# Optimization experiments

Measured on AMD Instinct MI355X. Metric: run time of the kernel, lower is better.

The kernel has to match this reference:

```python
import jax, jax.numpy as jnp
import numpy as np

jax.config.update("jax_enable_x64", True)

HLB_LVL_MAX = 20
HLB_LVL = 5
HLB_SHIFT = True
HLB_MAX = 2 ** HLB_LVL_MAX                      # 1048576
HLB_BIAS = (2 ** (HLB_LVL_MAX - HLB_LVL) - 1) if HLB_SHIFT else 0   # 32767
NUM_BITS = HLB_LVL_MAX + (1 if HLB_SHIFT else 0)  # 21 bits per axis, 63 total -> int64


def hilbert_encode3d(grd, num_bits):
    """Skilling's AxesToTranspose + bit interleave: 3D grid coords -> Hilbert order.
    grd: [..., 3] int64, coords < 2**num_bits. Returns int64 [...].
    Fixed-trip-count Python loops over bits (unrolled at trace time, ~21 iters)."""
    nd = 3
    x = [grd[..., i] for i in range(nd)]
    M = 1 << (num_bits - 1)
    # Inverse undo excess work
    Q = M
    while Q > 1:
        P = Q - 1
        for i in range(nd):
            cond = (x[i] & Q) != 0
            t = (x[0] ^ x[i]) & P
            new_x0 = jnp.where(cond, x[0] ^ P, x[0] ^ t)   # invert low bits of x0, or exchange
            new_xi = jnp.where(cond, x[i], x[i] ^ t)
            x[0] = new_x0
            if i != 0:
                x[i] = new_xi
        Q >>= 1
    # Gray encode
    for i in range(1, nd):
        x[i] = x[i] ^ x[i - 1]
    t = jnp.zeros_like(x[0])
    Q = M
    while Q > 1:
        t = jnp.where((x[nd - 1] & Q) != 0, t ^ (Q - 1), t)
        Q >>= 1
    for i in range(nd):
        x[i] = x[i] ^ t
    # Interleave bits of the transposed coords (x[0] most significant at each level)
    h = jnp.zeros_like(x[0])
    for b in range(num_bits):
        for i in range(nd):
            bit = (x[i] >> b) & 1
            h = h | (bit << (b * nd + (nd - 1 - i)))
    return h


def setup_inputs() -> dict:
    key = jax.random.key(0)
    z = jax.random.normal(key, (32, 131072, 3), dtype=jnp.float32)
    return {"z": z}


def reference(z):
    z = z.astype(jnp.float64)
    z_ce = z.mean(axis=1, keepdims=True)                                  # [B,1,3]
    r = jnp.sqrt(jnp.max(jnp.sum((z - z_ce) ** 2, axis=2), axis=1))       # [B]
    z_r = r[:, None, None] + 1e-6                                          # [B,1,1]
    z_nm = (z - z_ce + z_r) / (2.0 * z_r)                                  # normalized to ~[0,1]
    grd_idx = (HLB_MAX * z_nm).astype(jnp.int64) + HLB_BIAS                # quantize (trunc toward 0)
    hlb_ord = hilbert_encode3d(grd_idx, NUM_BITS)                          # [B,N] int64
    idx_pa = jnp.argsort(hlb_ord, axis=1)                                  # permutation along curve
    idx_re = jnp.argsort(idx_pa, axis=1)                                   # inverse permutation
    return idx_pa, idx_re
```

## Files before the change

kernel.cpp:

```cpp
#include <hip/hip_runtime.h>

typedef unsigned int u32;
typedef unsigned long long u64;
typedef unsigned short u16;

#define NB 32
#define NP 131072
#define THREADS 256
#define STHREADS 1024
#define RADIX 256
#define PASSES 6

#define SBPB 16
#define STILE 8192
#define SIPT 8
#define EBPB 64
#define ETILE 2048
#define EIPT 8


__device__ __forceinline__ u64 spread3(u32 v) {
    u64 x = (u64)(v & 0x1FFFFFu);
    x = (x | (x << 32)) & 0x001F00000000FFFFull;
    x = (x | (x << 16)) & 0x001F0000FF0000FFull;
    x = (x | (x << 8))  & 0x100F00F00F00F00Full;
    x = (x | (x << 4))  & 0x10C30C30C30C30C3ull;
    x = (x | (x << 2))  & 0x1249249249249249ull;
    return x;
}

__device__ __forceinline__ u64 hilbert3d(u32 x0, u32 x1, u32 x2) {
    #pragma unroll
    for (int q = 20; q >= 3; --q) {
        u32 Q = 1u << q, P = Q - 1u;
        if (x0 & Q) x0 ^= P;
        u32 t = (x0 ^ x1) & P;
        if (x1 & Q) { x0 ^= P; } else { x0 ^= t; x1 ^= t; }
        t = (x0 ^ x2) & P;
        if (x2 & Q) { x0 ^= P; } else { x0 ^= t; x2 ^= t; }
    }
    x1 ^= x0;
    x2 ^= x1;
    u32 y = x2;
    y ^= y >> 1; y ^= y >> 2; y ^= y >> 4; y ^= y >> 8; y ^= y >> 16;
    u32 t2 = y >> 1;
    x0 ^= t2; x1 ^= t2; x2 ^= t2;
    return (spread3(x0) << 2) | (spread3(x1) << 1) | spread3(x2);
}


__global__ __launch_bounds__(THREADS) void k_sum(const float* __restrict__ z,
                                                 double* __restrict__ partial) {
    int id = blockIdx.x;
    int b = (id & 7) * 4 + ((id >> 3) >> 6);
    int blk = (id >> 3) & 63;
    int tid = threadIdx.x;
    const float* zb = z + ((size_t)b * NP + (size_t)blk * ETILE) * 3;
    double s0 = 0.0, s1 = 0.0, s2 = 0.0;
    #pragma unroll
    for (int r = 0; r < EIPT; ++r) {
        int p = r * THREADS + tid;
        s0 += (double)zb[p * 3 + 0];
        s1 += (double)zb[p * 3 + 1];
        s2 += (double)zb[p * 3 + 2];
    }
    for (int off = 32; off > 0; off >>= 1) {
        s0 += __shfl_down(s0, off);
        s1 += __shfl_down(s1, off);
        s2 += __shfl_down(s2, off);
    }
    __shared__ double red[4][3];
    int lane = tid & 63, wave = tid >> 6;
    if (lane == 0) { red[wave][0] = s0; red[wave][1] = s1; red[wave][2] = s2; }
    __syncthreads();
    if (tid == 0) {
        size_t o = ((size_t)b * EBPB + blk) * 3;
        partial[o + 0] = red[0][0] + red[1][0] + red[2][0] + red[3][0];
        partial[o + 1] = red[0][1] + red[1][1] + red[2][1] + red[3][1];
        partial[o + 2] = red[0][2] + red[1][2] + red[2][2] + red[3][2];
    }
}

__global__ __launch_bounds__(THREADS) void k_maxp(const float* __restrict__ z,
                                                  const double* __restrict__ partial,
                                                  double* __restrict__ pmax) {
    int id = blockIdx.x;
    int b = (id & 7) * 4 + ((id >> 3) >> 6);
    int blk = (id >> 3) & 63;
    int tid = threadIdx.x;
    __shared__ double cS[3];
    if (tid < 64) {
        size_t o = ((size_t)b * EBPB + tid) * 3;
        double v0 = partial[o + 0], v1 = partial[o + 1], v2 = partial[o + 2];
        for (int off = 32; off > 0; off >>= 1) {
            v0 += __shfl_down(v0, off);
            v1 += __shfl_down(v1, off);
            v2 += __shfl_down(v2, off);
        }
        if (tid == 0) {
            cS[0] = v0 / (double)NP;
            cS[1] = v1 / (double)NP;
            cS[2] = v2 / (double)NP;
        }
    }
    __syncthreads();
    double c0 = cS[0], c1 = cS[1], c2 = cS[2];
    const float4* zb4 = (const float4*)(z + ((size_t)b * NP + (size_t)blk * ETILE) * 3);
    double m = 0.0;
    #pragma unroll
    for (int g = 0; g < 2; ++g) {
        int q4 = g * 768 + tid * 3;
        float4 va = zb4[q4 + 0], vb = zb4[q4 + 1], vc = zb4[q4 + 2];
        float px[4] = {va.x, va.w, vb.z, vc.y};
        float py[4] = {va.y, vb.x, vb.w, vc.z};
        float pz[4] = {va.z, vb.y, vc.x, vc.w};
        #pragma unroll
        for (int j = 0; j < 4; ++j) {
            double d0 = (double)px[j] - c0;
            double d1 = (double)py[j] - c1;
            double d2 = (double)pz[j] - c2;
            double s = (d0 * d0 + d1 * d1) + d2 * d2;
            m = fmax(m, s);
        }
    }
    for (int off = 32; off > 0; off >>= 1) m = fmax(m, __shfl_down(m, off));
    __shared__ double red[4];
    int lane = tid & 63, wave = tid >> 6;
    if (lane == 0) red[wave] = m;
    __syncthreads();
    if (tid == 0) pmax[(size_t)b * EBPB + blk] = fmax(fmax(red[0], red[1]), fmax(red[2], red[3]));
}


__device__ __forceinline__ void quant_prologue(const double* __restrict__ partial,
                                               const double* __restrict__ pmax,
                                               int b, int tid, double* nS) {
    if (tid < 64) {
        size_t o = ((size_t)b * EBPB + tid) * 3;
        double v0 = partial[o + 0], v1 = partial[o + 1], v2 = partial[o + 2];
        for (int off = 32; off > 0; off >>= 1) {
            v0 += __shfl_down(v0, off);
            v1 += __shfl_down(v1, off);
            v2 += __shfl_down(v2, off);
        }
        double m = pmax[(size_t)b * EBPB + tid];
        for (int off = 32; off > 0; off >>= 1) m = fmax(m, __shfl_down(m, off));
        if (tid == 0) {
            double zr = sqrt(m) + 1e-6;
            double A = 1048576.0 / (2.0 * zr);
            nS[0] = A;
            nS[1] = (zr - v0 / (double)NP) * A;
            nS[2] = (zr - v1 / (double)NP) * A;
            nS[3] = (zr - v2 / (double)NP) * A;
        }
    }
}

__global__ __launch_bounds__(THREADS) void k_encode(const float* __restrict__ z,
                                                    const double* __restrict__ partial,
                                                    const double* __restrict__ pmax,
                                                    u32* __restrict__ klo,
                                                    u32* __restrict__ khi,
                                                    u32* __restrict__ hist) {
    int id = blockIdx.x;
    int b = (id & 7) * 4 + ((id >> 3) >> 6);
    int blk = (id >> 3) & 63;
    int tid = threadIdx.x;
    __shared__ u32 lh[RADIX];
    __shared__ double nS[4];
    lh[tid] = 0;
    quant_prologue(partial, pmax, b, tid, nS);
    __syncthreads();
    double A = nS[0], B0 = nS[1], B1 = nS[2], B2 = nS[3];
    size_t batchBase = (size_t)b * NP;
    for (int r = 0; r < EIPT; ++r) {
        int p = blk * ETILE + r * THREADS + tid;
        size_t zi = (batchBase + p) * 3;
        u32 g0 = (u32)fma((double)z[zi + 0], A, B0) + 32767u;
        u32 g1 = (u32)fma((double)z[zi + 1], A, B1) + 32767u;
        u32 g2 = (u32)fma((double)z[zi + 2], A, B2) + 32767u;
        u64 key = hilbert3d(g0, g1, g2) >> 16;
        u32 lo = (u32)key;
        u32 hp = ((u32)(key >> 32) << 17) | (u32)p;
        klo[batchBase + p] = lo;
        khi[batchBase + p] = hp;
        atomicAdd(&lh[lo & 255u], 1u);
    }
    __syncthreads();
    hist[((size_t)b * RADIX + tid) * EBPB + blk] = lh[tid];
}

__device__ u32 g_lut[128];

__global__ __launch_bounds__(THREADS) void k_encode2(const float* __restrict__ z,
                                                     const double* __restrict__ partial,
                                                     const double* __restrict__ pmax,
                                                     u32* __restrict__ klo,
                                                     u32* __restrict__ khi,
                                                     u32* __restrict__ hist) {
    int id = blockIdx.x;
    int b = (id & 7) * 4 + ((id >> 3) >> 6);
    int blk = (id >> 3) & 63;
    int tid = threadIdx.x;
    __shared__ u32 lh[RADIX];
    __shared__ u32 ltw[128];
    __shared__ double nS[4];
    lh[tid] = 0;
    if (tid >= 128 && tid < 256) ltw[tid - 128] = g_lut[tid - 128];
    quant_prologue(partial, pmax, b, tid, nS);
    __syncthreads();
    const unsigned char* lt = (const unsigned char*)ltw;
    double A = nS[0], B0 = nS[1], B1 = nS[2], B2 = nS[3];
    size_t batchBase = (size_t)b * NP;
    const float4* zb4 = (const float4*)(z + (batchBase + (size_t)blk * ETILE) * 3);
    #pragma unroll
    for (int g = 0; g < 2; ++g) {
        int p0i = blk * ETILE + g * 1024 + tid * 4;
        int q4 = g * 768 + tid * 3;
        float4 va = zb4[q4 + 0], vb = zb4[q4 + 1], vc = zb4[q4 + 2];
        float px[4] = {va.x, va.w, vb.z, vc.y};
        float py[4] = {va.y, vb.x, vb.w, vc.z};
        float pz[4] = {va.z, vb.y, vc.x, vc.w};
        u32 g0[4], g1[4], g2[4];
        #pragma unroll
        for (int j = 0; j < 4; ++j) {
            g0[j] = (u32)fma((double)px[j], A, B0) + 32767u;
            g1[j] = (u32)fma((double)py[j], A, B1) + 32767u;
            g2[j] = (u32)fma((double)pz[j], A, B2) + 32767u;
        }
        u32 st[4] = {0u, 0u, 0u, 0u};
        u32 Hh[4] = {0u, 0u, 0u, 0u};
        u32 Hl[4] = {0u, 0u, 0u, 0u};
        #pragma unroll
        for (int l = 20; l >= 12; --l) {
            #pragma unroll
            for (int j = 0; j < 4; ++j) {
                u32 o = (((g0[j] >> l) & 1u) << 2) | (((g1[j] >> l) & 1u) << 1)
                      | ((g2[j] >> l) & 1u);
                u32 e = (u32)lt[st[j] | o];
                Hh[j] = (Hh[j] << 3) | (e & 7u);
                st[j] = e & 0xF8u;
            }
        }
        #pragma unroll
        for (int l = 11; l >= 2; --l) {
            #pragma unroll
            for (int j = 0; j < 4; ++j) {
                u32 o = (((g0[j] >> l) & 1u) << 2) | (((g1[j] >> l) & 1u) << 1)
                      | ((g2[j] >> l) & 1u);
                u32 e = (u32)lt[st[j] | o];
                Hl[j] = (Hl[j] << 3) | (e & 7u);
                st[j] = e & 0xF8u;
            }
        }
        u32 lo[4], hp[4];
        #pragma unroll
        for (int j = 0; j < 4; ++j) {
            lo[j] = (Hl[j] >> 10) | (Hh[j] << 20);
            hp[j] = ((Hh[j] >> 12) << 17) | (u32)(p0i + j);
            atomicAdd(&lh[lo[j] & 255u], 1u);
        }
        *(uint4*)(klo + batchBase + p0i) = make_uint4(lo[0], lo[1], lo[2], lo[3]);
        *(uint4*)(khi + batchBase + p0i) = make_uint4(hp[0], hp[1], hp[2], hp[3]);
    }
    __syncthreads();
    hist[((size_t)b * RADIX + tid) * EBPB + blk] = lh[tid];
}


__global__ __launch_bounds__(THREADS) void k_hist(const u32* __restrict__ dig,
                                                  u32* __restrict__ hist, int shift) {
    int id = blockIdx.x;
    int b = (id & 7) * 4 + ((id >> 3) >> 6);
    int blk = (id >> 3) & 63;
    int tid = threadIdx.x;
    __shared__ u32 lh[RADIX];
    lh[tid] = 0;
    __syncthreads();
    const uint4* dv = (const uint4*)(dig + (size_t)b * NP + (size_t)blk * ETILE);
    #pragma unroll
    for (int r = 0; r < EIPT / 4; ++r) {
        uint4 k = dv[r * THREADS + tid];
        atomicAdd(&lh[(k.x >> shift) & 255u], 1u);
        atomicAdd(&lh[(k.y >> shift) & 255u], 1u);
        atomicAdd(&lh[(k.z >> shift) & 255u], 1u);
        atomicAdd(&lh[(k.w >> shift) & 255u], 1u);
    }
    __syncthreads();
    hist[((size_t)b * RADIX + tid) * EBPB + blk] = lh[tid];
}


template<bool HAS_W1, bool OUT_W0, bool LAST>
__global__ __launch_bounds__(STHREADS, 8) void k_scatter(
    const u32* __restrict__ digIn,
    const u32* __restrict__ w1In,
    u32* __restrict__ w0Out, u32* __restrict__ w1Out,
    int* __restrict__ out0, int* __restrict__ out1,
    const u32* __restrict__ hist, int shiftW)
{
    int id = blockIdx.x;
    int b = (id & 7) * 4 + ((id >> 3) >> 4);
    int tile = (id >> 3) & 15;
    int tid = threadIdx.x, lane = tid & 63, wave = tid >> 6;

    __shared__ __align__(16) u32 sbuf[HAS_W1 ? 2 * STILE : STILE];
    __shared__ u16 wrun[16][RADIX];
    __shared__ u16 lstart[RADIX];
    __shared__ u32 baseS[RADIX];
    __shared__ u32 wsum[4];
    uint2* stage2 = reinterpret_cast<uint2*>(sbuf);
    u32* stage1 = sbuf;

    {
        int d2 = tid & 255, hw = (tid >> 8) * 4;
        wrun[hw + 0][d2] = 0; wrun[hw + 1][d2] = 0;
        wrun[hw + 2][d2] = 0; wrun[hw + 3][d2] = 0;
    }

    size_t batchBase = (size_t)b * NP;
    u32 tileOff = (u32)tile * STILE + (u32)wave * (STILE / 16);

    u32 w0[SIPT], w1v[SIPT], dr[SIPT];
    u64 lmask = (1ull << lane) - 1ull;

    #pragma unroll
    for (int it = 0; it < SIPT; ++it)
        w0[it] = digIn[batchBase + tileOff + it * 64 + lane];
    if (HAS_W1) {
        #pragma unroll
        for (int it = 0; it < SIPT; ++it)
            w1v[it] = w1In[batchBase + tileOff + it * 64 + lane];
    }

    u32 tot = 0, part = 0, vscan = 0;
    if (tid < 256) {
        const uint4* hp = (const uint4*)(hist + ((size_t)b * RADIX + tid) * EBPB);
        #pragma unroll
        for (int q = 0; q < EBPB / 4; ++q) {
            uint4 v = hp[q];
            u32 s4 = v.x + v.y + v.z + v.w;
            tot += s4;
            part += (q < tile) ? s4 : 0u;
        }
        vscan = tot;
        for (int off = 1; off < 64; off <<= 1) {
            u32 n = __shfl_up(vscan, off);
            if (lane >= off) vscan += n;
        }
        if (lane == 63) wsum[wave] = vscan;
    }
    __syncthreads();
    if (tid < 256) {
        u32 woff = 0;
        for (int w = 0; w < 4; ++w)
            if (w < wave) woff += wsum[w];
        baseS[tid] = woff + vscan - tot + part;
    }

    #pragma unroll
    for (int it = 0; it < SIPT; ++it) {
        u32 d = (w0[it] >> shiftW) & 255u;
        u64 m = ~0ull;
        #pragma unroll
        for (int bb = 0; bb < 8; ++bb) {
            u64 bal = __ballot((d >> bb) & 1u);
            m &= ((d >> bb) & 1u) ? bal : ~bal;
        }
        u32 lower = (u32)__popcll(m & lmask);
        u32 base = (u32)wrun[wave][d];
        if (lower == 0) wrun[wave][d] = (u16)(base + (u32)__popcll(m));
        dr[it] = (d << 16) | (base + lower);
    }
    __syncthreads();

    u32 cnt = 0, vs2 = 0;
    if (tid < 256) {
        u32 run = 0;
        #pragma unroll
        for (int w = 0; w < 16; ++w) { u32 c = wrun[w][tid]; wrun[w][tid] = (u16)run; run += c; }
        cnt = run;
        vs2 = cnt;
        for (int off = 1; off < 64; off <<= 1) {
            u32 n = __shfl_up(vs2, off);
            if (lane >= off) vs2 += n;
        }
        if (lane == 63) wsum[wave] = vs2;
    }
    __syncthreads();
    if (tid < 256) {
        u32 woff = 0;
        for (int w = 0; w < 4; ++w)
            if (w < wave) woff += wsum[w];
        lstart[tid] = (u16)(woff + vs2 - cnt);
    }
    __syncthreads();

    if (HAS_W1) {
        #pragma unroll
        for (int it = 0; it < SIPT; ++it) {
            u32 d = dr[it] >> 16, r = dr[it] & 0xFFFFu;
            u32 slot = (u32)lstart[d] + (u32)wrun[wave][d] + r;
            stage2[slot] = make_uint2(w0[it], w1v[it]);
        }
        __syncthreads();
        #pragma unroll
        for (int r = 0; r < SIPT; ++r) {
            int s = r * STHREADS + tid;
            uint2 kv = stage2[s];
            u32 d = (kv.x >> shiftW) & 255u;
            u32 pos = baseS[d] + (u32)s - (u32)lstart[d];
            if (OUT_W0) w0Out[batchBase + pos] = kv.x;
            w1Out[batchBase + pos] = kv.y;
        }
    } else {
        #pragma unroll
        for (int it = 0; it < SIPT; ++it) {
            u32 d = dr[it] >> 16, r = dr[it] & 0xFFFFu;
            u32 slot = (u32)lstart[d] + (u32)wrun[wave][d] + r;
            stage1[slot] = w0[it];
        }
        __syncthreads();
        #pragma unroll
        for (int r = 0; r < SIPT; ++r) {
            int s = r * STHREADS + tid;
            u32 k = stage1[s];
            u32 d = (k >> shiftW) & 255u;
            u32 pos = baseS[d] + (u32)s - (u32)lstart[d];
            if (LAST) {
                u32 idx = k & 0x1FFFFu;
                out0[batchBase + pos] = (int)idx;
                out1[batchBase + idx] = (int)pos;
            } else {
                w0Out[batchBase + pos] = k;
            }
        }
    }
}


namespace lut_build {

static u64 hfull(u32 a, u32 bcoord, u32 c) {
    u32 x[3] = {a, bcoord, c};
    const u32 M = 1u << 20;
    for (u32 Q = M; Q > 1; Q >>= 1) {
        u32 P = Q - 1u;
        for (int i = 0; i < 3; ++i) {
            if (x[i] & Q) x[0] ^= P;
            else { u32 t = (x[0] ^ x[i]) & P; x[0] ^= t; x[i] ^= t; }
        }
    }
    x[1] ^= x[0]; x[2] ^= x[1];
    u32 t = 0;
    for (u32 Q = M; Q > 1; Q >>= 1) if (x[2] & Q) t ^= (Q - 1u);
    x[0] ^= t; x[1] ^= t; x[2] ^= t;
    u64 h = 0;
    for (int bb = 0; bb < 21; ++bb)
        for (int i = 0; i < 3; ++i)
            h |= (u64)((x[i] >> bb) & 1u) << (bb * 3 + (2 - i));
    return h;
}

static int digit_at(u32 p0, u32 p1, u32 p2, int l) {
    return (int)((hfull(p0, p1, p2) >> (3 * l)) & 7u);
}

struct Sig { unsigned char v[72]; };

static bool sig_eq(const Sig& x, const Sig& y) {
    for (int i = 0; i < 72; ++i) if (x.v[i] != y.v[i]) return false;
    return true;
}

static void mk_sig(u32 c0, u32 c1, u32 c2, int l, Sig& s) {
    for (int o = 0; o < 8; ++o) {
        u32 p0 = c0 | ((u32)((o >> 2) & 1) << l);
        u32 p1 = c1 | ((u32)((o >> 1) & 1) << l);
        u32 p2 = c2 | ((u32)(o & 1) << l);
        s.v[o] = (unsigned char)digit_at(p0, p1, p2, l);
        for (int o2 = 0; o2 < 8; ++o2) {
            u32 q0 = p0 | ((u32)((o2 >> 2) & 1) << (l - 1));
            u32 q1 = p1 | ((u32)((o2 >> 1) & 1) << (l - 1));
            u32 q2 = p2 | ((u32)(o2 & 1) << (l - 1));
            s.v[8 + o * 8 + o2] = (unsigned char)digit_at(q0, q1, q2, l - 1);
        }
    }
}

static bool build(unsigned char* tab) {
    const int MAXS = 48;
    static Sig sigs[MAXS];
    struct Node { u32 c0, c1, c2; int l; };
    static Node nodes[MAXS];
    bool expanded[MAXS] = {false};
    int ns = 0;
    for (int i = 0; i < 512; ++i) tab[i] = 0;
    mk_sig(0, 0, 0, 20, sigs[0]);
    nodes[0] = {0, 0, 0, 20};
    ns = 1;
    bool progress = true;
    while (progress) {
        progress = false;
        for (int sI = 0; sI < ns; ++sI) {
            if (expanded[sI]) continue;
            Node n = nodes[sI];
            if (n.l < 2) return false;
            for (int o = 0; o < 8; ++o) {
                u32 p0 = n.c0 | ((u32)((o >> 2) & 1) << n.l);
                u32 p1 = n.c1 | ((u32)((o >> 1) & 1) << n.l);
                u32 p2 = n.c2 | ((u32)(o & 1) << n.l);
                int d = digit_at(p0, p1, p2, n.l);
                Sig cs; mk_sig(p0, p1, p2, n.l - 1, cs);
                int cid = -1;
                for (int k = 0; k < ns; ++k)
                    if (sig_eq(sigs[k], cs)) { cid = k; break; }
                if (cid < 0) {
                    if (ns >= MAXS) return false;
                    cid = ns;
                    sigs[ns] = cs;
                    nodes[ns] = {p0, p1, p2, n.l - 1};
                    ns++;
                }
                if (cid >= 32) return false;
                tab[sI * 8 + o] = (unsigned char)(d | (cid << 3));
            }
            expanded[sI] = true;
            progress = true;
        }
    }
    u64 rng = 0x9E3779B97F4A7C15ull;
    for (int it = 0; it < 6008; ++it) {
        u32 p0, p1, p2;
        if (it < 8) {
            p0 = (it & 4) ? 0x1FFFFFu : 0u;
            p1 = (it & 2) ? 0x1FFFFFu : 0u;
            p2 = (it & 1) ? 0x1FFFFFu : 0u;
        } else {
            rng ^= rng << 13; rng ^= rng >> 7; rng ^= rng << 17; p0 = (u32)(rng & 0x1FFFFFu);
            rng ^= rng << 13; rng ^= rng >> 7; rng ^= rng << 17; p1 = (u32)(rng & 0x1FFFFFu);
            rng ^= rng << 13; rng ^= rng >> 7; rng ^= rng << 17; p2 = (u32)(rng & 0x1FFFFFu);
        }
        u32 s8 = 0, Hh = 0, Hl = 0;
        for (int l = 20; l >= 12; --l) {
            u32 o = (((p0 >> l) & 1u) << 2) | (((p1 >> l) & 1u) << 1) | ((p2 >> l) & 1u);
            u32 e = tab[s8 | o];
            Hh = (Hh << 3) | (e & 7u);
            s8 = e & 0xF8u;
        }
        for (int l = 11; l >= 2; --l) {
            u32 o = (((p0 >> l) & 1u) << 2) | (((p1 >> l) & 1u) << 1) | ((p2 >> l) & 1u);
            u32 e = tab[s8 | o];
            Hl = (Hl << 3) | (e & 7u);
            s8 = e & 0xF8u;
        }
        u32 lo = (Hl >> 10) | (Hh << 20);
        u32 hi15 = Hh >> 12;
        u64 key = ((u64)hi15 << 32) | (u64)lo;
        if (key != (hfull(p0, p1, p2) >> 16)) return false;
    }
    return true;
}

}

static unsigned char h_tab[512];

struct LutInit {
    bool ok;
    void* dev;
    LutInit() : ok(false), dev(nullptr) {
        ok = lut_build::build(h_tab);
        if (ok) {
            if (hipGetSymbolAddress(&dev, HIP_SYMBOL(g_lut)) != hipSuccess || dev == nullptr)
                ok = false;
        }
    }
};


extern "C" void kernel_launch(void* const* d_in, const int* in_sizes, int n_in,
                              void* d_out, int out_size, void* d_ws, size_t ws_size,
                              hipStream_t stream) {
    const float* z = (const float*)d_in[0];
    int* out0 = (int*)d_out;
    int* out1 = out0 + (size_t)NB * NP;

    char* ws = (char*)d_ws;
    u32* loA  = (u32*)(ws + 0);
    u32* hiA  = (u32*)(ws + 16777216);
    u32* loB  = (u32*)(ws + 33554432);
    u32* hiB  = (u32*)(ws + 50331648);
    u32* hist = (u32*)(ws + 67108864);
    double* partial = (double*)(ws + 69206016);
    double* pmax    = (double*)(ws + 69255168);

    static LutInit li;

    const int egrid = NB * EBPB;
    const int sgrid = NB * SBPB;

    if (li.ok) {
        hipMemcpyAsync(li.dev, h_tab, 512, hipMemcpyHostToDevice, stream);
    }

    k_sum<<<egrid, THREADS, 0, stream>>>(z, partial);
    k_maxp<<<egrid, THREADS, 0, stream>>>(z, partial, pmax);
    if (li.ok) {
        k_encode2<<<egrid, THREADS, 0, stream>>>(z, partial, pmax, loA, hiA, hist);
    } else {
        k_encode<<<egrid, THREADS, 0, stream>>>(z, partial, pmax, loA, hiA, hist);
    }

    k_scatter<true,  true,  false><<<sgrid, STHREADS, 0, stream>>>(
        loA, hiA, loB, hiB, nullptr, nullptr, hist, 0);
    k_hist<<<egrid, THREADS, 0, stream>>>(loB, hist, 8);
    k_scatter<true,  true,  false><<<sgrid, STHREADS, 0, stream>>>(
        loB, hiB, loA, hiA, nullptr, nullptr, hist, 8);
    k_hist<<<egrid, THREADS, 0, stream>>>(loA, hist, 16);
    k_scatter<true,  true,  false><<<sgrid, STHREADS, 0, stream>>>(
        loA, hiA, loB, hiB, nullptr, nullptr, hist, 16);
    k_hist<<<egrid, THREADS, 0, stream>>>(loB, hist, 24);
    k_scatter<true,  false, false><<<sgrid, STHREADS, 0, stream>>>(
        loB, hiB, nullptr, hiA, nullptr, nullptr, hist, 24);
    k_hist<<<egrid, THREADS, 0, stream>>>(hiA, hist, 17);
    k_scatter<false, true,  false><<<sgrid, STHREADS, 0, stream>>>(
        hiA, nullptr, hiB, nullptr, nullptr, nullptr, hist, 17);
    k_hist<<<egrid, THREADS, 0, stream>>>(hiB, hist, 25);
    k_scatter<false, false, true ><<<sgrid, STHREADS, 0, stream>>>(
        hiB, nullptr, nullptr, nullptr, out0, out1, hist, 25);
}
```

Measured before the change: 298.3 us.

## Fuse next-pass digit histogram into radix scatter and drop separate histogram kernels

Each scatter pass now builds the histogram for the next radix digit from its output positions in shared memory. It adds the counts into a per-tile (16-tile) global histogram with atomics, which removes the five k_hist launches and their full key re-reads. Histograms use a coarser tile granularity matching the scatter tiles, and each pass gets its own buffer, zeroed once by a new kernel. This trades launches and memory traffic for extra shared-memory atomics, global atomics and syncs inside the scatter kernel.

```diff
diff --git a/kernel.cpp b/kernel.cpp
--- a/kernel.cpp
+++ b/kernel.cpp
@@ -11,12 +11,16 @@
 #define RADIX 256
 #define PASSES 6
 
+
 #define SBPB 16
 #define STILE 8192
 #define SIPT 8
 #define EBPB 64
 #define ETILE 2048
 #define EIPT 8
+
+#define HT 16
+#define HS1 (NB * RADIX * HT)
 
 
 __device__ __forceinline__ u64 spread3(u32 v) {
@@ -46,6 +50,14 @@
     u32 t2 = y >> 1;
     x0 ^= t2; x1 ^= t2; x2 ^= t2;
     return (spread3(x0) << 2) | (spread3(x1) << 1) | spread3(x2);
+}
+
+
+__global__ __launch_bounds__(THREADS) void k_zero(uint4* __restrict__ p) {
+    int gid = blockIdx.x * THREADS + threadIdx.x;
+    #pragma unroll
+    for (int r = 0; r < 4; ++r)
+        p[(size_t)r * 49152 + gid] = make_uint4(0u, 0u, 0u, 0u);
 }
 
 
@@ -187,7 +199,7 @@
         atomicAdd(&lh[lo & 255u], 1u);
     }
     __syncthreads();
-    hist[((size_t)b * RADIX + tid) * EBPB + blk] = lh[tid];
+    atomicAdd(&hist[((size_t)b * RADIX + tid) * HT + (blk >> 2)], lh[tid]);
 }
 
 __device__ u32 g_lut[128];
@@ -264,40 +276,19 @@
         *(uint4*)(khi + batchBase + p0i) = make_uint4(hp[0], hp[1], hp[2], hp[3]);
     }
     __syncthreads();
-    hist[((size_t)b * RADIX + tid) * EBPB + blk] = lh[tid];
-}
-
-
-__global__ __launch_bounds__(THREADS) void k_hist(const u32* __restrict__ dig,
-                                                  u32* __restrict__ hist, int shift) {
-    int id = blockIdx.x;
-    int b = (id & 7) * 4 + ((id >> 3) >> 6);
-    int blk = (id >> 3) & 63;
-    int tid = threadIdx.x;
-    __shared__ u32 lh[RADIX];
-    lh[tid] = 0;
-    __syncthreads();
-    const uint4* dv = (const uint4*)(dig + (size_t)b * NP + (size_t)blk * ETILE);
-    #pragma unroll
-    for (int r = 0; r < EIPT / 4; ++r) {
-        uint4 k = dv[r * THREADS + tid];
-        atomicAdd(&lh[(k.x >> shift) & 255u], 1u);
-        atomicAdd(&lh[(k.y >> shift) & 255u], 1u);
-        atomicAdd(&lh[(k.z >> shift) & 255u], 1u);
-        atomicAdd(&lh[(k.w >> shift) & 255u], 1u);
-    }
-    __syncthreads();
-    hist[((size_t)b * RADIX + tid) * EBPB + blk] = lh[tid];
-}
-
-
-template<bool HAS_W1, bool OUT_W0, bool LAST>
+    atomicAdd(&hist[((size_t)b * RADIX + tid) * HT + (blk >> 2)], lh[tid]);
+}
+
+
+template<bool HAS_W1, bool OUT_W0, bool LAST, int NEXTSH, bool NEXTW1>
 __global__ __launch_bounds__(STHREADS, 8) void k_scatter(
     const u32* __restrict__ digIn,
     const u32* __restrict__ w1In,
     u32* __restrict__ w0Out, u32* __restrict__ w1Out,
     int* __restrict__ out0, int* __restrict__ out1,
-    const u32* __restrict__ hist, int shiftW)
+    const u32* __restrict__ hist,
+    u32* __restrict__ histNext,
+    int shiftW)
 {
     int id = blockIdx.x;
     int b = (id & 7) * 4 + ((id >> 3) >> 4);
@@ -335,13 +326,14 @@
 
     u32 tot = 0, part = 0, vscan = 0;
     if (tid < 256) {
-        const uint4* hp = (const uint4*)(hist + ((size_t)b * RADIX + tid) * EBPB);
-        #pragma unroll
-        for (int q = 0; q < EBPB / 4; ++q) {
+        const uint4* hp = (const uint4*)(hist + ((size_t)b * RADIX + tid) * HT);
+        #pragma unroll
+        for (int q = 0; q < HT / 4; ++q) {
             uint4 v = hp[q];
-            u32 s4 = v.x + v.y + v.z + v.w;
-            tot += s4;
-            part += (q < tile) ? s4 : 0u;
+            int t0 = q * 4;
+            tot += v.x + v.y + v.z + v.w;
+            part += (t0 + 0 < tile ? v.x : 0u) + (t0 + 1 < tile ? v.y : 0u)
+                  + (t0 + 2 < tile ? v.z : 0u) + (t0 + 3 < tile ? v.w : 0u);
         }
         vscan = tot;
         for (int off = 1; off < 64; off <<= 1) {
@@ -396,6 +388,7 @@
     }
     __syncthreads();
 
+    u32 pn[SIPT];
     if (HAS_W1) {
         #pragma unroll
         for (int it = 0; it < SIPT; ++it) {
@@ -412,6 +405,8 @@
             u32 pos = baseS[d] + (u32)s - (u32)lstart[d];
             if (OUT_W0) w0Out[batchBase + pos] = kv.x;
             w1Out[batchBase + pos] = kv.y;
+            if (NEXTSH >= 0)
+                pn[r] = ((((NEXTW1 ? kv.y : kv.x) >> NEXTSH) & 255u) << 17) | pos;
         }
     } else {
         #pragma unroll
@@ -433,7 +428,28 @@
                 out1[batchBase + idx] = (int)pos;
             } else {
                 w0Out[batchBase + pos] = k;
+                if (NEXTSH >= 0)
+                    pn[r] = (((k >> NEXTSH) & 255u) << 17) | pos;
             }
+        }
+    }
+
+    if (NEXTSH >= 0) {
+        __syncthreads();
+        u32* dh = sbuf;
+        #pragma unroll
+        for (int c = 0; c < 4; ++c) dh[c * STHREADS + tid] = 0;
+        __syncthreads();
+        #pragma unroll
+        for (int r = 0; r < SIPT; ++r)
+            atomicAdd(&dh[((pn[r] & 0x1FFFFu) >> 13) * 256 + (pn[r] >> 17)], 1u);
+        __syncthreads();
+        #pragma unroll
+        for (int c = 0; c < 4; ++c) {
+            int cell = c * STHREADS + tid;
+            u32 v = dh[cell];
+            if (v) atomicAdd(&histNext[((size_t)b * RADIX + (cell & 255)) * HT
+                                       + (cell >> 8)], v);
         }
     }
 }
@@ -587,13 +603,13 @@
     int* out1 = out0 + (size_t)NB * NP;
 
     char* ws = (char*)d_ws;
-    u32* loA  = (u32*)(ws + 0);
-    u32* hiA  = (u32*)(ws + 16777216);
-    u32* loB  = (u32*)(ws + 33554432);
-    u32* hiB  = (u32*)(ws + 50331648);
-    u32* hist = (u32*)(ws + 67108864);
-    double* partial = (double*)(ws + 69206016);
-    double* pmax    = (double*)(ws + 69255168);
+    u32* loA   = (u32*)(ws + 0);
+    u32* hiA   = (u32*)(ws + 16777216);
+    u32* loB   = (u32*)(ws + 33554432);
+    u32* hiB   = (u32*)(ws + 50331648);
+    u32* histS = (u32*)(ws + 67108864);
+    double* partial = (double*)(ws + 70254592);
+    double* pmax    = (double*)(ws + 70303744);
 
     static LutInit li;
 
@@ -603,30 +619,27 @@
     if (li.ok) {
         hipMemcpyAsync(li.dev, h_tab, 512, hipMemcpyHostToDevice, stream);
     }
+
+    k_zero<<<192, THREADS, 0, stream>>>((uint4*)histS);
 
     k_sum<<<egrid, THREADS, 0, stream>>>(z, partial);
     k_maxp<<<egrid, THREADS, 0, stream>>>(z, partial, pmax);
     if (li.ok) {
-        k_encode2<<<egrid, THREADS, 0, stream>>>(z, partial, pmax, loA, hiA, hist);
+        k_encode2<<<egrid, THREADS, 0, stream>>>(z, partial, pmax, loA, hiA, histS);
     } else {
-        k_encode<<<egrid, THREADS, 0, stream>>>(z, partial, pmax, loA, hiA, hist);
-    }
-
-    k_scatter<true,  true,  false><<<sgrid, STHREADS, 0, stream>>>(
-        loA, hiA, loB, hiB, nullptr, nullptr, hist, 0);
-    k_hist<<<egrid, THREADS, 0, stream>>>(loB, hist, 8);
-    k_scatter<true,  true,  false><<<sgrid, STHREADS, 0, stream>>>(
-        loB, hiB, loA, hiA, nullptr, nullptr, hist, 8);
-    k_hist<<<egrid, THREADS, 0, stream>>>(loA, hist, 16);
-    k_scatter<true,  true,  false><<<sgrid, STHREADS, 0, stream>>>(
-        loA, hiA, loB, hiB, nullptr, nullptr, hist, 16);
-    k_hist<<<egrid, THREADS, 0, stream>>>(loB, hist, 24);
-    k_scatter<true,  false, false><<<sgrid, STHREADS, 0, stream>>>(
-        loB, hiB, nullptr, hiA, nullptr, nullptr, hist, 24);
-    k_hist<<<egrid, THREADS, 0, stream>>>(hiA, hist, 17);
-    k_scatter<false, true,  false><<<sgrid, STHREADS, 0, stream>>>(
-        hiA, nullptr, hiB, nullptr, nullptr, nullptr, hist, 17);
-    k_hist<<<egrid, THREADS, 0, stream>>>(hiB, hist, 25);
-    k_scatter<false, false, true ><<<sgrid, STHREADS, 0, stream>>>(
-        hiB, nullptr, nullptr, nullptr, out0, out1, hist, 25);
-}
+        k_encode<<<egrid, THREADS, 0, stream>>>(z, partial, pmax, loA, hiA, histS);
+    }
+
+    k_scatter<true,  true,  false, 8,  false><<<sgrid, STHREADS, 0, stream>>>(
+        loA, hiA, loB, hiB, nullptr, nullptr, histS + 0 * HS1, histS + 1 * HS1, 0);
+    k_scatter<true,  true,  false, 16, false><<<sgrid, STHREADS, 0, stream>>>(
+        loB, hiB, loA, hiA, nullptr, nullptr, histS + 1 * HS1, histS + 2 * HS1, 8);
+    k_scatter<true,  true,  false, 24, false><<<sgrid, STHREADS, 0, stream>>>(
+        loA, hiA, loB, hiB, nullptr, nullptr, histS + 2 * HS1, histS + 3 * HS1, 16);
+    k_scatter<true,  false, false, 17, true ><<<sgrid, STHREADS, 0, stream>>>(
+        loB, hiB, nullptr, hiA, nullptr, nullptr, histS + 3 * HS1, histS + 4 * HS1, 24);
+    k_scatter<false, true,  false, 25, false><<<sgrid, STHREADS, 0, stream>>>(
+        hiA, nullptr, hiB, nullptr, nullptr, nullptr, histS + 4 * HS1, histS + 5 * HS1, 17);
+    k_scatter<false, false, true,  -1, false><<<sgrid, STHREADS, 0, stream>>>(
+        hiB, nullptr, nullptr, nullptr, out0, out1, histS + 5 * HS1, nullptr, 25);
+}
```

Result: slower. 526.3 us (+76.4%).
